# Performance work log

Hardware: AMD Instinct MI355X
Metric: run time of the kernel (lower is better)

The kernel has to match this reference:

```python
import jax, jax.numpy as jnp
import numpy as np

EPS = 1e-6

def setup_inputs() -> dict:
    key = jax.random.key(0)
    k1, k2, k3 = jax.random.split(key, 3)
    B, N, D, K = 8, 4096, 512, 8
    x = jax.random.normal(k1, (B, N, D), dtype=jnp.float32)
    W = jax.random.normal(k2, (D, K), dtype=jnp.float32) * (1.0 / np.sqrt(D))
    b = jnp.zeros((K,), dtype=jnp.float32)
    eps = jax.random.normal(k3, (B, K, D), dtype=jnp.float32)
    return {"x": x, "W": W, "b": b, "eps": eps}

def reference(x, W, b, eps):
    # x: [B,N,D], W: [D,K], b: [K], eps: [B,K,D]
    logits = jnp.einsum('bnd,dk->bnk', x, W) + b          # [B,N,K]
    probs = jax.nn.softmax(logits, axis=-1)               # softmax over clusters
    p = jnp.swapaxes(probs, 1, 2)                         # [B,K,N]
    # weighted sums (NOT normalized over N, matching the original)
    mu_k = jnp.einsum('bkn,bnd->bkd', p, x)               # [B,K,D]
    diff = x[:, None, :, :] - mu_k[:, :, None, :]         # [B,K,N,D]
    sigma_k = jnp.einsum('bkn,bknd->bkd', p, diff * diff) # [B,K,D]
    z_k = mu_k + eps * jnp.sqrt(sigma_k + EPS)            # reparameterization
    kl = -0.5 * jnp.sum(1.0 + jnp.log(sigma_k + EPS) - mu_k * mu_k - sigma_k, axis=-1)  # [B,K]
    kl_loss = jnp.mean(kl)
    pooled_z = jnp.mean(z_k, axis=1)                      # [B,D]
    return pooled_z, kl_loss
```

## Files before the change

### kernel.cpp

```cpp
#include <hip/hip_runtime.h>


typedef float v2f __attribute__((ext_vector_type(2)));

#define B_ 8
#define N_ 4096
#define D_ 512
#define K_ 8
#define EPS_ 1e-6f
#define CHUNKS 32
#define WAVES 8
#define ROWS_PER_WAVE 16


__global__ __launch_bounds__(512, 2)
void k1_accum(const float* __restrict__ x, const float* __restrict__ W,
              const float* __restrict__ bias, float* __restrict__ ws,
              int cstride, int atomic_mode) {
  const int lane = threadIdx.x & 63;
  const int wave = threadIdx.x >> 6;
  const int b    = blockIdx.x >> 5;
  const int chunk= blockIdx.x & 31;
  const int m    = lane & 7;

  const int d0 = lane * 4;

  v2f wk[8][4];
#pragma unroll
  for (int c = 0; c < 4; ++c) {
    const float4* wr0 = reinterpret_cast<const float4*>(&W[(d0 + c) * K_]);
    float4 wa = wr0[0], wb = wr0[1];
    wk[c][0] = (v2f){wa.x, wa.y}; wk[c][1] = (v2f){wa.z, wa.w};
    wk[c][2] = (v2f){wb.x, wb.y}; wk[c][3] = (v2f){wb.z, wb.w};
    const float4* wr1 = reinterpret_cast<const float4*>(&W[(256 + d0 + c) * K_]);
    float4 wc = wr1[0], wd = wr1[1];
    wk[4+c][0] = (v2f){wc.x, wc.y}; wk[4+c][1] = (v2f){wc.z, wc.w};
    wk[4+c][2] = (v2f){wd.x, wd.y}; wk[4+c][3] = (v2f){wd.z, wd.w};
  }
  const float biasv = bias[m];

  v2f acc[8][8];
#pragma unroll
  for (int dj = 0; dj < 8; ++dj)
#pragma unroll
    for (int k = 0; k < 8; ++k) acc[dj][k] = (v2f){0.f, 0.f};
  float s0acc = 0.f;

  const bool c0 = (lane & 1) != 0;
  const bool c1 = (lane & 2) != 0;
  const bool c2 = (lane & 4) != 0;

  const int row_base = chunk * (WAVES * ROWS_PER_WAVE) + wave * ROWS_PER_WAVE;
  const float* xb = x + (size_t)b * N_ * D_;

  const float4* xr = reinterpret_cast<const float4*>(&xb[(size_t)row_base * D_]);
  float4 xa = xr[lane];
  float4 xc = xr[64 + lane];

  for (int i = 0; i < ROWS_PER_WAVE; ++i) {
    const int nrow = row_base + ((i + 1 < ROWS_PER_WAVE) ? i + 1 : i);
    const float4* xrn = reinterpret_cast<const float4*>(&xb[(size_t)nrow * D_]);
    float4 na = xrn[lane];
    float4 nc = xrn[64 + lane];

    float xv[8] = {xa.x, xa.y, xa.z, xa.w, xc.x, xc.y, xc.z, xc.w};

    v2f qp[4] = {(v2f){0,0},(v2f){0,0},(v2f){0,0},(v2f){0,0}};
#pragma unroll
    for (int dj = 0; dj < 8; ++dj) {
      v2f xx = (v2f){xv[dj], xv[dj]};
#pragma unroll
      for (int kp = 0; kp < 4; ++kp) qp[kp] += wk[dj][kp] * xx;
    }
    float q0=qp[0].x,q1=qp[0].y,q2=qp[1].x,q3=qp[1].y;
    float q4=qp[2].x,q5=qp[2].y,q6=qp[3].x,q7=qp[3].y;

    float r0 = c0 ? q0 : q1, r1 = c0 ? q2 : q3, r2 = c0 ? q4 : q5, r3 = c0 ? q6 : q7;
    r0 = __shfl_xor(r0, 1, 64); r1 = __shfl_xor(r1, 1, 64);
    r2 = __shfl_xor(r2, 1, 64); r3 = __shfl_xor(r3, 1, 64);
    float a0 = (c0 ? q1 : q0) + r0, a1 = (c0 ? q3 : q2) + r1;
    float a2 = (c0 ? q5 : q4) + r2, a3 = (c0 ? q7 : q6) + r3;
    float s0g = c1 ? a0 : a1, s1g = c1 ? a2 : a3;
    s0g = __shfl_xor(s0g, 2, 64); s1g = __shfl_xor(s1g, 2, 64);
    float b0 = (c1 ? a1 : a0) + s0g, b1 = (c1 ? a3 : a2) + s1g;
    float g0 = c2 ? b0 : b1;
    g0 = __shfl_xor(g0, 4, 64);
    float t = (c2 ? b1 : b0) + g0;
    t += __shfl_xor(t, 8, 64);
    t += __shfl_xor(t, 16, 64);
    t += __shfl_xor(t, 32, 64);
    t += biasv;

    float mx = fmaxf(t, __shfl_xor(t, 1, 64));
    mx = fmaxf(mx, __shfl_xor(mx, 2, 64));
    mx = fmaxf(mx, __shfl_xor(mx, 4, 64));
    float e = __expf(t - mx);
    float se = e + __shfl_xor(e, 1, 64);
    se += __shfl_xor(se, 2, 64);
    se += __shfl_xor(se, 4, 64);
    float pm = e * __builtin_amdgcn_rcpf(se);
    s0acc += pm;

    float p[8];
#define GATH(KK) p[KK] = __int_as_float(__builtin_amdgcn_ds_swizzle(__float_as_int(pm), ((KK) << 5) | 0x18))
    GATH(0); GATH(1); GATH(2); GATH(3); GATH(4); GATH(5); GATH(6); GATH(7);
#undef GATH

#pragma unroll
    for (int dj = 0; dj < 8; ++dj) {
      v2f m2 = (v2f){xv[dj], xv[dj] * xv[dj]};
#pragma unroll
      for (int k = 0; k < 8; ++k) {
        v2f pp = (v2f){p[k], p[k]};
        acc[dj][k] += m2 * pp;
      }
    }

    xa = na; xc = nc;
  }

  float* partial = ws;
  float* s0p = ws + (size_t)B_ * cstride * K_ * D_ * 2;
  const int cslot = atomic_mode ? 0 : chunk;

  __shared__ float s0sh[WAVES][K_];
  __shared__ v2f sh[WAVES][2][K_][64];

  if (lane < K_) s0sh[wave][lane] = s0acc;
  __syncthreads();
  if (threadIdx.x < K_) {
    float s = 0.f;
#pragma unroll
    for (int w = 0; w < WAVES; ++w) s += s0sh[w][threadIdx.x];
    float* dst = s0p + (size_t)(b * cstride + cslot) * K_ + threadIdx.x;
    if (atomic_mode) atomicAdd(dst, s); else *dst = s;
  }

#pragma unroll
  for (int r = 0; r < 4; ++r) {
#pragma unroll
    for (int k = 0; k < 8; ++k) {
      sh[wave][0][k][lane] = acc[2*r][k];
      sh[wave][1][k][lane] = acc[2*r + 1][k];
    }
    __syncthreads();
    v2f sA = sh[0][0][wave][lane];
    v2f sB = sh[0][1][wave][lane];
#pragma unroll
    for (int w = 1; w < WAVES; ++w) {
      sA += sh[w][0][wave][lane];
      sB += sh[w][1][wave][lane];
    }
    const int d = (r < 2) ? (lane * 4 + 2 * r) : (256 + lane * 4 + (2 * r - 4));
    float* dst = partial + (((size_t)(b * cstride + cslot) * K_ + wave) * D_ + d) * 2;
    if (atomic_mode) {
      atomicAdd(dst + 0, sA.x); atomicAdd(dst + 1, sA.y);
      atomicAdd(dst + 2, sB.x); atomicAdd(dst + 3, sB.y);
    } else {
      float4 v; v.x = sA.x; v.y = sA.y; v.z = sB.x; v.w = sB.y;
      *reinterpret_cast<float4*>(dst) = v;
    }
    __syncthreads();
  }
}

__global__ __launch_bounds__(128)
void k2_final(const float* __restrict__ ws, const float* __restrict__ eps,
              float* __restrict__ out, int cstride, int nchunks) {
  const int b = blockIdx.x >> 5;
  const int slice = blockIdx.x & 31;
  const int tid = threadIdx.x;
  const int k = tid >> 4;
  const int dl = tid & 15;
  const int d = slice * 16 + dl;

  const float* partial = ws;
  const float* s0p = ws + (size_t)B_ * cstride * K_ * D_ * 2;

  __shared__ float s0sh[K_];
  __shared__ float zsh[K_][16];
  __shared__ float klsh[2];

  if (tid < K_) {
    float s = 0.f;
    for (int c = 0; c < nchunks; ++c) s += s0p[(size_t)(b * cstride + c) * K_ + tid];
    s0sh[tid] = s;
  }
  __syncthreads();

  float S1 = 0.f, S2 = 0.f;
  for (int c = 0; c < nchunks; ++c) {
    const v2f v = *reinterpret_cast<const v2f*>(
        partial + (((size_t)(b * cstride + c) * K_ + k) * D_ + d) * 2);
    S1 += v.x; S2 += v.y;
  }
  const float S0 = s0sh[k];
  float sigraw = S2 + (S0 - 2.f) * S1 * S1;
  float sig = fmaxf(sigraw, 0.f) + EPS_;
  float z = S1 + eps[((size_t)(b * K_ + k)) * D_ + d] * sqrtf(sig);
  zsh[k][dl] = z;
  float klp = 1.f + logf(sig) - S1 * S1 - sigraw;

  klp += __shfl_xor(klp, 1, 64);
  klp += __shfl_xor(klp, 2, 64);
  klp += __shfl_xor(klp, 4, 64);
  klp += __shfl_xor(klp, 8, 64);
  klp += __shfl_xor(klp, 16, 64);
  klp += __shfl_xor(klp, 32, 64);
  const int lane = tid & 63, wv = tid >> 6;
  if (lane == 0) klsh[wv] = klp;
  __syncthreads();

  if (tid < 16) {
    float pooled = 0.f;
#pragma unroll
    for (int kk = 0; kk < K_; ++kk) pooled += zsh[kk][tid];
    out[b * D_ + slice * 16 + tid] = pooled * 0.125f;
  }
  if (tid == 0) {
    atomicAdd(out + B_ * D_, (klsh[0] + klsh[1]) * (-0.5f / (B_ * K_)));
  }
}

extern "C" void kernel_launch(void* const* d_in, const int* in_sizes, int n_in,
                              void* d_out, int out_size, void* d_ws, size_t ws_size,
                              hipStream_t stream) {
  const float* x    = (const float*)d_in[0];
  const float* W    = (const float*)d_in[1];
  const float* bias = (const float*)d_in[2];
  const float* eps  = (const float*)d_in[3];
  float* out = (float*)d_out;
  float* ws  = (float*)d_ws;

  const size_t full_floats = (size_t)B_ * CHUNKS * K_ * D_ * 2 + (size_t)B_ * CHUNKS * K_;
  const int atomic_mode = (ws_size < full_floats * sizeof(float)) ? 1 : 0;
  const int cstride = atomic_mode ? 1 : CHUNKS;
  const int nchunks = atomic_mode ? 1 : CHUNKS;

  if (atomic_mode) {
    const size_t zbytes = ((size_t)B_ * 1 * K_ * D_ * 2 + (size_t)B_ * 1 * K_) * sizeof(float);
    hipMemsetAsync(ws, 0, zbytes, stream);
  }
  hipMemsetAsync(out + B_ * D_, 0, sizeof(float), stream);

  k1_accum<<<B_ * CHUNKS, 64 * WAVES, 0, stream>>>(x, W, bias, ws, cstride, atomic_mode);
  k2_final<<<B_ * CHUNKS, 128, 0, stream>>>(ws, eps, out, cstride, nchunks);
}
```

Measured before the change: 49.64 us.

## Split fused accumulation into separate softmax-probability and moment kernels

Result: slower. 61.25 us (+23.4%).

```diff
diff --git a/kernel.cpp b/kernel.cpp
--- a/kernel.cpp
+++ b/kernel.cpp
@@ -12,18 +12,20 @@
 #define WAVES 8
 #define ROWS_PER_WAVE 16
 
+#define P_FLOATS ((size_t)B_ * N_ * K_)
 
 __global__ __launch_bounds__(512, 2)
-void k1_accum(const float* __restrict__ x, const float* __restrict__ W,
-              const float* __restrict__ bias, float* __restrict__ ws,
-              int cstride, int atomic_mode) {
+void kA_probs(const float* __restrict__ x, const float* __restrict__ W,
+              const float* __restrict__ bias, float* __restrict__ P,
+              float* __restrict__ s0p, int cstride, int atomic_mode) {
+#pragma clang fp contract(fast)
   const int lane = threadIdx.x & 63;
   const int wave = threadIdx.x >> 6;
   const int b    = blockIdx.x >> 5;
   const int chunk= blockIdx.x & 31;
   const int m    = lane & 7;
-
-  const int d0 = lane * 4;
+  const int grp  = lane >> 3;
+  const int d0   = lane * 4;
 
   v2f wk[8][4];
 #pragma unroll
@@ -39,102 +41,131 @@
   }
   const float biasv = bias[m];
 
-  v2f acc[8][8];
-#pragma unroll
-  for (int dj = 0; dj < 8; ++dj)
-#pragma unroll
-    for (int k = 0; k < 8; ++k) acc[dj][k] = (v2f){0.f, 0.f};
-  float s0acc = 0.f;
-
   const bool c0 = (lane & 1) != 0;
   const bool c1 = (lane & 2) != 0;
   const bool c2 = (lane & 4) != 0;
 
   const int row_base = chunk * (WAVES * ROWS_PER_WAVE) + wave * ROWS_PER_WAVE;
   const float* xb = x + (size_t)b * N_ * D_;
-
-  const float4* xr = reinterpret_cast<const float4*>(&xb[(size_t)row_base * D_]);
-  float4 xa = xr[lane];
-  float4 xc = xr[64 + lane];
-
-  for (int i = 0; i < ROWS_PER_WAVE; ++i) {
-    const int nrow = row_base + ((i + 1 < ROWS_PER_WAVE) ? i + 1 : i);
-    const float4* xrn = reinterpret_cast<const float4*>(&xb[(size_t)nrow * D_]);
-    float4 na = xrn[lane];
-    float4 nc = xrn[64 + lane];
-
-    float xv[8] = {xa.x, xa.y, xa.z, xa.w, xc.x, xc.y, xc.z, xc.w};
-
-    v2f qp[4] = {(v2f){0,0},(v2f){0,0},(v2f){0,0},(v2f){0,0}};
-#pragma unroll
-    for (int dj = 0; dj < 8; ++dj) {
-      v2f xx = (v2f){xv[dj], xv[dj]};
-#pragma unroll
-      for (int kp = 0; kp < 4; ++kp) qp[kp] += wk[dj][kp] * xx;
-    }
-    float q0=qp[0].x,q1=qp[0].y,q2=qp[1].x,q3=qp[1].y;
-    float q4=qp[2].x,q5=qp[2].y,q6=qp[3].x,q7=qp[3].y;
-
-    float r0 = c0 ? q0 : q1, r1 = c0 ? q2 : q3, r2 = c0 ? q4 : q5, r3 = c0 ? q6 : q7;
-    r0 = __shfl_xor(r0, 1, 64); r1 = __shfl_xor(r1, 1, 64);
-    r2 = __shfl_xor(r2, 1, 64); r3 = __shfl_xor(r3, 1, 64);
-    float a0 = (c0 ? q1 : q0) + r0, a1 = (c0 ? q3 : q2) + r1;
-    float a2 = (c0 ? q5 : q4) + r2, a3 = (c0 ? q7 : q6) + r3;
-    float s0g = c1 ? a0 : a1, s1g = c1 ? a2 : a3;
-    s0g = __shfl_xor(s0g, 2, 64); s1g = __shfl_xor(s1g, 2, 64);
-    float b0 = (c1 ? a1 : a0) + s0g, b1 = (c1 ? a3 : a2) + s1g;
-    float g0 = c2 ? b0 : b1;
-    g0 = __shfl_xor(g0, 4, 64);
-    float t = (c2 ? b1 : b0) + g0;
-    t += __shfl_xor(t, 8, 64);
-    t += __shfl_xor(t, 16, 64);
-    t += __shfl_xor(t, 32, 64);
-    t += biasv;
-
-    float mx = fmaxf(t, __shfl_xor(t, 1, 64));
-    mx = fmaxf(mx, __shfl_xor(mx, 2, 64));
-    mx = fmaxf(mx, __shfl_xor(mx, 4, 64));
-    float e = __expf(t - mx);
-    float se = e + __shfl_xor(e, 1, 64);
-    se += __shfl_xor(se, 2, 64);
-    se += __shfl_xor(se, 4, 64);
-    float pm = e * __builtin_amdgcn_rcpf(se);
-    s0acc += pm;
-
-    float p[8];
-#define GATH(KK) p[KK] = __int_as_float(__builtin_amdgcn_ds_swizzle(__float_as_int(pm), ((KK) << 5) | 0x18))
-    GATH(0); GATH(1); GATH(2); GATH(3); GATH(4); GATH(5); GATH(6); GATH(7);
-#undef GATH
-
-#pragma unroll
-    for (int dj = 0; dj < 8; ++dj) {
-      v2f m2 = (v2f){xv[dj], xv[dj] * xv[dj]};
-#pragma unroll
-      for (int k = 0; k < 8; ++k) {
-        v2f pp = (v2f){p[k], p[k]};
-        acc[dj][k] += m2 * pp;
+  float* Pb = P + ((size_t)b * N_ + row_base) * K_;
+
+  float s0acc = 0.f;
+
+  for (int batch = 0; batch < 2; ++batch) {
+    float psel = 0.f;
+#pragma unroll
+    for (int j = 0; j < 8; ++j) {
+      const int row = row_base + batch * 8 + j;
+      const float4* xr = reinterpret_cast<const float4*>(&xb[(size_t)row * D_]);
+      float4 xa = xr[lane];
+      float4 xc = xr[64 + lane];
+      float xv[8] = {xa.x, xa.y, xa.z, xa.w, xc.x, xc.y, xc.z, xc.w};
+
+      v2f qp[4] = {(v2f){0,0},(v2f){0,0},(v2f){0,0},(v2f){0,0}};
+#pragma unroll
+      for (int dj = 0; dj < 8; ++dj) {
+        v2f xx = (v2f){xv[dj], xv[dj]};
+#pragma unroll
+        for (int kp = 0; kp < 4; ++kp) qp[kp] += wk[dj][kp] * xx;
       }
-    }
-
-    xa = na; xc = nc;
-  }
-
-  float* partial = ws;
-  float* s0p = ws + (size_t)B_ * cstride * K_ * D_ * 2;
-  const int cslot = atomic_mode ? 0 : chunk;
+      float q0=qp[0].x,q1=qp[0].y,q2=qp[1].x,q3=qp[1].y;
+      float q4=qp[2].x,q5=qp[2].y,q6=qp[3].x,q7=qp[3].y;
+
+      float r0 = c0 ? q0 : q1, r1 = c0 ? q2 : q3, r2 = c0 ? q4 : q5, r3 = c0 ? q6 : q7;
+      r0 = __shfl_xor(r0, 1, 64); r1 = __shfl_xor(r1, 1, 64);
+      r2 = __shfl_xor(r2, 1, 64); r3 = __shfl_xor(r3, 1, 64);
+      float a0 = (c0 ? q1 : q0) + r0, a1 = (c0 ? q3 : q2) + r1;
+      float a2 = (c0 ? q5 : q4) + r2, a3 = (c0 ? q7 : q6) + r3;
+      float s0g = c1 ? a0 : a1, s1g = c1 ? a2 : a3;
+      s0g = __shfl_xor(s0g, 2, 64); s1g = __shfl_xor(s1g, 2, 64);
+      float b0 = (c1 ? a1 : a0) + s0g, b1 = (c1 ? a3 : a2) + s1g;
+      float g0 = c2 ? b0 : b1;
+      g0 = __shfl_xor(g0, 4, 64);
+      float t = (c2 ? b1 : b0) + g0;
+      t += __shfl_xor(t, 8, 64);
+      t += __shfl_xor(t, 16, 64);
+      t += __shfl_xor(t, 32, 64);
+      t += biasv;
+
+      float mx = fmaxf(t, __shfl_xor(t, 1, 64));
+      mx = fmaxf(mx, __shfl_xor(mx, 2, 64));
+      mx = fmaxf(mx, __shfl_xor(mx, 4, 64));
+      float e = __expf(t - mx);
+      float se = e + __shfl_xor(e, 1, 64);
+      se += __shfl_xor(se, 2, 64);
+      se += __shfl_xor(se, 4, 64);
+      float pm = e * __builtin_amdgcn_rcpf(se);
+
+      s0acc += pm;
+      psel = (grp == j) ? pm : psel;
+    }
+    Pb[batch * 64 + lane] = psel;
+  }
 
   __shared__ float s0sh[WAVES][K_];
-  __shared__ v2f sh[WAVES][2][K_][64];
-
   if (lane < K_) s0sh[wave][lane] = s0acc;
   __syncthreads();
   if (threadIdx.x < K_) {
     float s = 0.f;
 #pragma unroll
     for (int w = 0; w < WAVES; ++w) s += s0sh[w][threadIdx.x];
+    const int cslot = atomic_mode ? 0 : chunk;
     float* dst = s0p + (size_t)(b * cstride + cslot) * K_ + threadIdx.x;
     if (atomic_mode) atomicAdd(dst, s); else *dst = s;
   }
+}
+
+__global__ __launch_bounds__(512, 2)
+void kB_moments(const float* __restrict__ x, const float* __restrict__ P,
+                float* __restrict__ partial, int cstride, int atomic_mode) {
+#pragma clang fp contract(fast)
+  const int lane = threadIdx.x & 63;
+  const int wave = threadIdx.x >> 6;
+  const int b    = blockIdx.x >> 5;
+  const int chunk= blockIdx.x & 31;
+
+  v2f acc[8][8];
+#pragma unroll
+  for (int dj = 0; dj < 8; ++dj)
+#pragma unroll
+    for (int k = 0; k < 8; ++k) acc[dj][k] = (v2f){0.f, 0.f};
+
+  const int row_base = chunk * (WAVES * ROWS_PER_WAVE) + wave * ROWS_PER_WAVE;
+  const float* xb = x + (size_t)b * N_ * D_;
+  const float* Prow = P + ((size_t)b * N_ + row_base) * K_;
+
+  const float4* xr = reinterpret_cast<const float4*>(&xb[(size_t)row_base * D_]);
+  float4 xa = xr[lane];
+  float4 xc = xr[64 + lane];
+  const float4* pr = reinterpret_cast<const float4*>(Prow);
+  float4 pA = pr[0], pB = pr[1];
+
+  for (int i = 0; i < ROWS_PER_WAVE; ++i) {
+    const int ni = (i + 1 < ROWS_PER_WAVE) ? i + 1 : i;
+    const float4* xrn = reinterpret_cast<const float4*>(&xb[(size_t)(row_base + ni) * D_]);
+    float4 na = xrn[lane];
+    float4 nc = xrn[64 + lane];
+    const float4* prn = reinterpret_cast<const float4*>(Prow + (size_t)ni * K_);
+    float4 npA = prn[0], npB = prn[1];
+
+    float xv[8] = {xa.x, xa.y, xa.z, xa.w, xc.x, xc.y, xc.z, xc.w};
+    float pk[8] = {pA.x, pA.y, pA.z, pA.w, pB.x, pB.y, pB.z, pB.w};
+
+#pragma unroll
+    for (int dj = 0; dj < 8; ++dj) {
+      v2f m2 = (v2f){xv[dj], xv[dj] * xv[dj]};
+#pragma unroll
+      for (int k = 0; k < 8; ++k) {
+        v2f pp = (v2f){pk[k], pk[k]};
+        acc[dj][k] += m2 * pp;
+      }
+    }
+
+    xa = na; xc = nc; pA = npA; pB = npB;
+  }
+
+  const int cslot = atomic_mode ? 0 : chunk;
+  __shared__ v2f sh[WAVES][2][K_][64];
 
 #pragma unroll
   for (int r = 0; r < 4; ++r) {
@@ -165,17 +196,15 @@
 }
 
 __global__ __launch_bounds__(128)
-void k2_final(const float* __restrict__ ws, const float* __restrict__ eps,
-              float* __restrict__ out, int cstride, int nchunks) {
+void k2_final(const float* __restrict__ partial, const float* __restrict__ s0p,
+              const float* __restrict__ eps, float* __restrict__ out,
+              int cstride, int nchunks) {
   const int b = blockIdx.x >> 5;
   const int slice = blockIdx.x & 31;
   const int tid = threadIdx.x;
   const int k = tid >> 4;
   const int dl = tid & 15;
   const int d = slice * 16 + dl;
-
-  const float* partial = ws;
-  const float* s0p = ws + (size_t)B_ * cstride * K_ * D_ * 2;
 
   __shared__ float s0sh[K_];
   __shared__ float zsh[K_][16];
@@ -232,17 +261,24 @@
   float* out = (float*)d_out;
   float* ws  = (float*)d_ws;
 
-  const size_t full_floats = (size_t)B_ * CHUNKS * K_ * D_ * 2 + (size_t)B_ * CHUNKS * K_;
+  const size_t full_floats =
+      P_FLOATS + (size_t)B_ * CHUNKS * K_ * D_ * 2 + (size_t)B_ * CHUNKS * K_;
   const int atomic_mode = (ws_size < full_floats * sizeof(float)) ? 1 : 0;
   const int cstride = atomic_mode ? 1 : CHUNKS;
   const int nchunks = atomic_mode ? 1 : CHUNKS;
 
+  float* P       = ws;
+  float* partial = ws + P_FLOATS;
+  float* s0p     = partial + (size_t)B_ * cstride * K_ * D_ * 2;
+
   if (atomic_mode) {
-    const size_t zbytes = ((size_t)B_ * 1 * K_ * D_ * 2 + (size_t)B_ * 1 * K_) * sizeof(float);
-    hipMemsetAsync(ws, 0, zbytes, stream);
+    const size_t zbytes =
+        ((size_t)B_ * K_ * D_ * 2 + (size_t)B_ * K_) * sizeof(float);
+    hipMemsetAsync(partial, 0, zbytes, stream);
   }
   hipMemsetAsync(out + B_ * D_, 0, sizeof(float), stream);
 
-  k1_accum<<<B_ * CHUNKS, 64 * WAVES, 0, stream>>>(x, W, bias, ws, cstride, atomic_mode);
-  k2_final<<<B_ * CHUNKS, 128, 0, stream>>>(ws, eps, out, cstride, nchunks);
-}
+  kA_probs  <<<B_ * CHUNKS, 64 * WAVES, 0, stream>>>(x, W, bias, P, s0p, cstride, atomic_mode);
+  kB_moments<<<B_ * CHUNKS, 64 * WAVES, 0, stream>>>(x, P, partial, cstride, atomic_mode);
+  k2_final  <<<B_ * 32, 128, 0, stream>>>(partial, s0p, eps, out, cstride, nchunks);
+}
```
